# Kernel tuning notes

Measured on AMD Instinct MI355X. Metric: run time of the kernel, lower is better.

Reference implementation:

```python
import jax, jax.numpy as jnp
import numpy as np

B, N_LEAVES, HID, NCLS, VOCAB = 32, 512, 128, 2, 50257
N_NODES = 2 * N_LEAVES - 1  # complete binary tree, heap layout


def setup_inputs() -> dict:
    key = jax.random.key(0)
    ks = jax.random.split(key, 12)
    x = jax.random.randint(ks[0], (B, N_NODES), 0, VOCAB)
    cue = jax.random.randint(ks[1], (B, N_NODES), 0, NCLS)
    # word j sits at tree leaf node L-1+j
    word_index = jnp.tile(jnp.arange(N_LEAVES - 1, 2 * N_LEAVES - 1), (B, 1))
    # parent->child adjacency stored in adj[:, 1]
    A = np.zeros((2, N_NODES, N_NODES), dtype=bool)
    p = np.arange(N_LEAVES - 1)
    A[1, p, 2 * p + 1] = True
    A[1, p, 2 * p + 2] = True
    adj = jnp.asarray(np.broadcast_to(A, (B, 2, N_NODES, N_NODES)).copy())
    s = 0.05
    emb = jax.random.normal(ks[2], (VOCAB, HID - NCLS)) * s
    Wc = jax.random.normal(ks[3], (HID, 2 * HID)) * s
    bc = jax.random.normal(ks[4], (HID,)) * s
    Wd = jax.random.normal(ks[5], (2 * HID, 2 * HID)) * s
    bd = jax.random.normal(ks[6], (2 * HID,)) * s
    Wg = jax.random.normal(ks[7], (HID, HID)) * s
    bg = jax.random.normal(ks[8], (HID,)) * s
    Wcl = jax.random.normal(ks[9], (NCLS, 2 * HID)) * s
    bcl = jax.random.normal(ks[10], (NCLS,)) * s
    return dict(x=x, word_index=word_index, cue=cue, adj=adj, emb=emb,
                Wc=Wc, bc=bc, Wd=Wd, bd=bd, Wg=Wg, bg=bg, Wcl=Wcl, bcl=bcl)


def reference(x, word_index, cue, adj, emb, Wc, bc, Wd, bd, Wg, bg, Wcl, bcl):
    # adj encodes the same complete binary heap tree that is hardcoded below
    Bn, N = x.shape
    H = Wc.shape[0]
    C = bcl.shape[0]
    L = (N + 1) // 2
    depth = L.bit_length() - 1  # leaves live at level `depth`
    bidx = jnp.arange(Bn)[:, None]

    word_emb = emb[x]                                   # (B, N, H-C)
    cue_oh = jax.nn.one_hot(cue, C, dtype=word_emb.dtype)
    in_feats = jnp.concatenate([word_emb, cue_oh], -1)  # (B, N, H)
    sent = in_feats[bidx, word_index]                   # (B, L, H) leaf feats

    # ---- upward compose: level-batched bottom-up traversal ----
    h = jnp.zeros((Bn, N, H), in_feats.dtype).at[bidx, word_index].set(sent)
    for d in range(depth - 1, -1, -1):
        p = jnp.arange(2 ** d - 1, 2 ** (d + 1) - 1)
        ctx = jnp.concatenate([h[:, 2 * p + 1], h[:, 2 * p + 2]], -1)  # (B, 2^d, 2H)
        h = h.at[:, p].set(jnp.tanh(ctx @ Wc.T + bc))
    # upward_results never writes leaf rows -> leaves stay zero
    up = h.at[bidx, word_index].set(0.0)

    g_down = jax.nn.sigmoid(h[:, 0] @ Wg.T + bg)        # (B, H)

    # ---- downward decompose: level-batched top-down traversal ----
    down = jnp.zeros_like(h).at[:, 0].set(g_down)
    for d in range(depth):
        p = jnp.arange(2 ** d - 1, 2 ** (d + 1) - 1)
        ctx = jnp.concatenate([down[:, p], up[:, p]], -1)
        ch = jnp.tanh(ctx @ Wd.T + bd)                  # (B, 2^d, 2H)
        down = down.at[:, 2 * p + 1].set(ch[..., :H]).at[:, 2 * p + 2].set(ch[..., H:])

    tree = jnp.concatenate([down, up], -1)              # (B, N, 2H)
    scores = jax.nn.sigmoid(tree @ Wcl.T + bcl)
    return jax.nn.softmax(scores, -1)
```

## Files before the change

kernel.cpp:

```cpp
#include <hip/hip_runtime.h>


constexpr int NNODES = 1023;
constexpr int HB = 128;

__device__ __forceinline__ float fold16(const float* a, int l) {
  float b[8];
#pragma unroll
  for (int u = 0; u < 8; ++u) {
    const float mine = (l & 1) ? a[2 * u + 1] : a[2 * u];
    const float oth  = (l & 1) ? a[2 * u]     : a[2 * u + 1];
    b[u] = mine + __shfl_xor(oth, 1);
  }
  float c[4];
#pragma unroll
  for (int u = 0; u < 4; ++u) {
    const float mine = (l & 2) ? b[2 * u + 1] : b[2 * u];
    const float oth  = (l & 2) ? b[2 * u]     : b[2 * u + 1];
    c[u] = mine + __shfl_xor(oth, 2);
  }
  float d[2];
#pragma unroll
  for (int u = 0; u < 2; ++u) {
    const float mine = (l & 4) ? c[2 * u + 1] : c[2 * u];
    const float oth  = (l & 4) ? c[2 * u]     : c[2 * u + 1];
    d[u] = mine + __shfl_xor(oth, 4);
  }
  const float mine = (l & 8) ? d[1] : d[0];
  const float oth  = (l & 8) ? d[0] : d[1];
  return mine + __shfl_xor(oth, 8);
}

__device__ __forceinline__ float fold8(const float* a, int l) {
  float b[4];
#pragma unroll
  for (int u = 0; u < 4; ++u) {
    const float mine = (l & 1) ? a[2 * u + 1] : a[2 * u];
    const float oth  = (l & 1) ? a[2 * u]     : a[2 * u + 1];
    b[u] = mine + __shfl_xor(oth, 1);
  }
  float c[2];
#pragma unroll
  for (int u = 0; u < 2; ++u) {
    const float mine = (l & 2) ? b[2 * u + 1] : b[2 * u];
    const float oth  = (l & 2) ? b[2 * u]     : b[2 * u + 1];
    c[u] = mine + __shfl_xor(oth, 2);
  }
  const float mine = (l & 4) ? c[1] : c[0];
  const float oth  = (l & 4) ? c[0] : c[1];
  return mine + __shfl_xor(oth, 4);
}

__device__ __forceinline__ float fold4(const float* a, int l) {
  float b[2];
#pragma unroll
  for (int u = 0; u < 2; ++u) {
    const float mine = (l & 1) ? a[2 * u + 1] : a[2 * u];
    const float oth  = (l & 1) ? a[2 * u]     : a[2 * u + 1];
    b[u] = mine + __shfl_xor(oth, 1);
  }
  const float mine = (l & 2) ? b[1] : b[0];
  const float oth  = (l & 2) ? b[0] : b[1];
  return mine + __shfl_xor(oth, 2);
}

template<int CH>
__device__ __forceinline__ float foldCH(const float (&a)[CH * 4], int l16) {
  if constexpr (CH == 4) {
    return fold16(a, l16);
  } else if constexpr (CH == 2) {
    float t = fold8(a, l16);
    t += __shfl_xor(t, 8);
    return t;
  } else {
    float t = fold4(a, l16);
    t += __shfl_xor(t, 4);
    t += __shfl_xor(t, 8);
    return t;
  }
}

template<int CH>
__device__ __forceinline__ void up_pass(float* __restrict__ heap, int base, int cb,
                                        int cbase, const float4 (&w)[4][4],
                                        float bias_r, int g, int l16, bool wr) {
  float a[CH * 4];
#pragma unroll
  for (int v = 0; v < CH * 4; ++v) a[v] = 0.f;
#pragma unroll
  for (int p = 0; p < CH; ++p) {
    const float* cp = heap + (cb + 2 * (cbase + p)) * HB + l16 * 4;
#pragma unroll
    for (int m = 0; m < 4; ++m) {
      const float4 cc = *(const float4*)(cp + m * 64);
#pragma unroll
      for (int r = 0; r < 4; ++r) {
        const float4 wv = w[r][m];
        a[p * 4 + r] = fmaf(wv.x, cc.x, fmaf(wv.y, cc.y,
                        fmaf(wv.z, cc.z, fmaf(wv.w, cc.w, a[p * 4 + r]))));
      }
    }
  }
  const float tot = foldCH<CH>(a, l16);
  if (wr && l16 < CH * 4) {
    const int p = l16 >> 2;
    heap[(base + cbase + p) * HB + 4 * g + (l16 & 3)] = tanhf(tot + bias_r);
  }
}

template<int NP, int NH>
__device__ __forceinline__ void up_level16(float* __restrict__ heap,
                                           const float4 (&w)[4][4],
                                           float bias_r, int g, int l16, int ph) {
  constexpr int base = NP - 1, cb = 2 * NP - 1;
  if constexpr (NP >= 4 * NH) {
#pragma unroll
    for (int c0 = 0; c0 < NP; c0 += 4 * NH)
      up_pass<4>(heap, base, cb, c0 + ph * 4, w, bias_r, g, l16, true);
  } else if constexpr (NP * 2 == 4 * NH) {
    up_pass<2>(heap, base, cb, ph * 2, w, bias_r, g, l16, true);
  } else if constexpr (NP == NH) {
    up_pass<1>(heap, base, cb, ph, w, bias_r, g, l16, true);
  } else {
    up_pass<1>(heap, base, cb, 0, w, bias_r, g, l16, ph == 0);
  }
  __syncthreads();
}

template<int CH>
__device__ __forceinline__ void down_pass(float* __restrict__ db,
                                          const float* __restrict__ ub,
                                          int base, int cb, int cbase,
                                          const float4 (&w)[4][4],
                                          float bias_r, int g, int l16) {
  float a[CH * 4];
#pragma unroll
  for (int v = 0; v < CH * 4; ++v) a[v] = 0.f;
#pragma unroll
  for (int p = 0; p < CH; ++p) {
    const float* dp = db + (base + cbase + p) * HB + l16 * 4;
    const float* up = ub + (base + cbase + p) * HB + l16 * 4;
#pragma unroll
    for (int m = 0; m < 4; ++m) {
      const float4 cc = *(const float4*)(((m < 2) ? dp : up) + (m & 1) * 64);
#pragma unroll
      for (int r = 0; r < 4; ++r) {
        const float4 wv = w[r][m];
        a[p * 4 + r] = fmaf(wv.x, cc.x, fmaf(wv.y, cc.y,
                        fmaf(wv.z, cc.z, fmaf(wv.w, cc.w, a[p * 4 + r]))));
      }
    }
  }
  const float tot = foldCH<CH>(a, l16);
  if (l16 < CH * 4) {
    const int p = l16 >> 2;
    const int row = 4 * g + (l16 & 3);
    db[(cb + 2 * (cbase + p) + (row >> 7)) * HB + (row & 127)] = tanhf(tot + bias_r);
  }
}

template<int NP>
__device__ __forceinline__ void down_level16(float* __restrict__ db,
                                             const float* __restrict__ ub,
                                             const float4 (&w)[4][4],
                                             float bias_r, int g, int l16) {
  constexpr int base = NP - 1, cb = 2 * NP - 1;
  if constexpr (NP >= 4) {
#pragma unroll
    for (int c0 = 0; c0 < NP; c0 += 4)
      down_pass<4>(db, ub, base, cb, c0, w, bias_r, g, l16);
  } else {
    down_pass<NP>(db, ub, base, cb, 0, w, bias_r, g, l16);
  }
  __syncthreads();
}

__device__ __forceinline__ void classify16(const float* __restrict__ dn,
                                           const float* __restrict__ un,
                                           const float* __restrict__ wcl,
                                           const float* __restrict__ bcl,
                                           float* __restrict__ o, int l16) {
  const int k0 = l16 * 8;
  float s0, s1;
  {
    const float4 d0 = *(const float4*)(dn + k0);
    const float4 d1 = *(const float4*)(dn + k0 + 4);
    const float4 a0 = *(const float4*)(wcl + k0);
    const float4 a1 = *(const float4*)(wcl + k0 + 4);
    const float4 b0 = *(const float4*)(wcl + 256 + k0);
    const float4 b1 = *(const float4*)(wcl + 256 + k0 + 4);
    s0 = d0.x * a0.x + d0.y * a0.y + d0.z * a0.z + d0.w * a0.w
       + d1.x * a1.x + d1.y * a1.y + d1.z * a1.z + d1.w * a1.w;
    s1 = d0.x * b0.x + d0.y * b0.y + d0.z * b0.z + d0.w * b0.w
       + d1.x * b1.x + d1.y * b1.y + d1.z * b1.z + d1.w * b1.w;
  }
  if (un) {
    const float4 u0 = *(const float4*)(un + k0);
    const float4 u1 = *(const float4*)(un + k0 + 4);
    const float4 a0 = *(const float4*)(wcl + 128 + k0);
    const float4 a1 = *(const float4*)(wcl + 128 + k0 + 4);
    const float4 b0 = *(const float4*)(wcl + 384 + k0);
    const float4 b1 = *(const float4*)(wcl + 384 + k0 + 4);
    s0 += u0.x * a0.x + u0.y * a0.y + u0.z * a0.z + u0.w * a0.w
        + u1.x * a1.x + u1.y * a1.y + u1.z * a1.z + u1.w * a1.w;
    s1 += u0.x * b0.x + u0.y * b0.y + u0.z * b0.z + u0.w * b0.w
        + u1.x * b1.x + u1.y * b1.y + u1.z * b1.z + u1.w * b1.w;
  }
#pragma unroll
  for (int m = 8; m >= 1; m >>= 1) {
    s0 += __shfl_xor(s0, m);
    s1 += __shfl_xor(s1, m);
  }
  if (l16 == 0) {
    s0 += bcl[0]; s1 += bcl[1];
    const float p0 = 1.f / (1.f + expf(-s0));
    const float p1 = 1.f / (1.f + expf(-s1));
    const float mx = fmaxf(p0, p1);
    const float e0 = expf(p0 - mx), e1 = expf(p1 - mx);
    const float inv = 1.f / (e0 + e1);
    o[0] = e0 * inv;
    o[1] = e1 * inv;
  }
}

__global__ __launch_bounds__(512, 4) void kA_up(const int* __restrict__ x,
                                                const int* __restrict__ cue,
                                                const float* __restrict__ emb,
                                                const float* __restrict__ Wc,
                                                const float* __restrict__ bc,
                                                float* __restrict__ hw) {
  __shared__ __align__(16) float heap[63 * HB];
  __shared__ __align__(16) float pad[7296];
  const int b = blockIdx.x >> 4, s = blockIdx.x & 15, r = 15 + s;
  const int t = threadIdx.x, g = t >> 4, l16 = t & 15;
  if (t == 0) ((volatile float*)pad)[0] = 0.f;

  float4 w[4][4];
#pragma unroll
  for (int rr = 0; rr < 4; ++rr)
#pragma unroll
    for (int m = 0; m < 4; ++m)
      w[rr][m] = *(const float4*)(Wc + (4 * g + rr) * 256 + l16 * 4 + m * 64);
  const float bias_r = bc[4 * g + (l16 & 3)];

  for (int idx = t; idx < 32 * HB; idx += 512) {
    const int j = idx >> 7, k = idx & 127;
    const int gq = ((r + 1) << 5) - 1 + j;
    float v;
    if (k < 126) v = emb[(long long)x[b * NNODES + gq] * 126 + k];
    else         v = (cue[b * NNODES + gq] == (k - 126)) ? 1.f : 0.f;
    heap[(31 + j) * HB + k] = v;
  }
  __syncthreads();

  up_level16<16, 1>(heap, w, bias_r, g, l16, 0);
  up_level16<8, 1>(heap, w, bias_r, g, l16, 0);
  up_level16<4, 1>(heap, w, bias_r, g, l16, 0);
  up_level16<2, 1>(heap, w, bias_r, g, l16, 0);
  up_level16<1, 1>(heap, w, bias_r, g, l16, 0);

  float4* dst = (float4*)(hw + (size_t)(b * 16 + s) * 31 * HB);
  const float4* src = (const float4*)heap;
  for (int idx = t; idx < 31 * 32; idx += 512) dst[idx] = src[idx];
}

__global__ __launch_bounds__(1024, 4) void kB_mid(const float* __restrict__ Wc,
                                                  const float* __restrict__ bc,
                                                  const float* __restrict__ Wg,
                                                  const float* __restrict__ bg,
                                                  const float* __restrict__ Wd,
                                                  const float* __restrict__ bd,
                                                  const float* __restrict__ Wcl,
                                                  const float* __restrict__ bcl,
                                                  const float* __restrict__ hw,
                                                  float* __restrict__ dw,
                                                  float* __restrict__ out) {
  __shared__ __align__(16) float ub[31 * HB];
  __shared__ __align__(16) float db[31 * HB];
  __shared__ __align__(16) float pad[12084];
  __shared__ __align__(16) float wcl[512];
  const int b = blockIdx.x, t = threadIdx.x;
  if (t == 0) ((volatile float*)pad)[0] = 0.f;

  {
    float4* u4 = (float4*)(ub + 15 * HB);
    for (int idx = t; idx < 16 * 32; idx += 1024) {
      const int s = idx >> 5, k4 = idx & 31;
      u4[idx] = ((const float4*)(hw + (size_t)(b * 16 + s) * 31 * HB))[k4];
    }
  }
  if (t < 512) wcl[t] = Wcl[t];
  __syncthreads();

  {
    const int g = (t >> 4) & 31, l16 = t & 15, ph = t >> 9;
    float4 w[4][4];
#pragma unroll
    for (int rr = 0; rr < 4; ++rr)
#pragma unroll
      for (int m = 0; m < 4; ++m)
        w[rr][m] = *(const float4*)(Wc + (4 * g + rr) * 256 + l16 * 4 + m * 64);
    const float bias_r = bc[4 * g + (l16 & 3)];
    up_level16<8, 2>(ub, w, bias_r, g, l16, ph);
    up_level16<4, 2>(ub, w, bias_r, g, l16, ph);
    up_level16<2, 2>(ub, w, bias_r, g, l16, ph);
    up_level16<1, 2>(ub, w, bias_r, g, l16, ph);

    float4 wg[4][2];
#pragma unroll
    for (int rr = 0; rr < 4; ++rr)
#pragma unroll
      for (int m = 0; m < 2; ++m)
        wg[rr][m] = *(const float4*)(Wg + (4 * g + rr) * 128 + l16 * 4 + m * 64);
    float a[4];
#pragma unroll
    for (int v = 0; v < 4; ++v) a[v] = 0.f;
#pragma unroll
    for (int m = 0; m < 2; ++m) {
      const float4 cc = *(const float4*)(ub + l16 * 4 + m * 64);
#pragma unroll
      for (int rr = 0; rr < 4; ++rr) {
        const float4 wv = wg[rr][m];
        a[rr] = fmaf(wv.x, cc.x, fmaf(wv.y, cc.y, fmaf(wv.z, cc.z, fmaf(wv.w, cc.w, a[rr]))));
      }
    }
    float tot = fold4(a, l16);
    tot += __shfl_xor(tot, 4);
    tot += __shfl_xor(tot, 8);
    if (ph == 0 && l16 < 4) {
      const int row = 4 * g + l16;
      db[row] = 1.f / (1.f + expf(-(tot + bg[row])));
    }
    __syncthreads();
  }
  asm volatile("" ::: "memory");

  {
    const int g = t >> 4, l16 = t & 15;
    float4 w[4][4];
#pragma unroll
    for (int rr = 0; rr < 4; ++rr)
#pragma unroll
      for (int m = 0; m < 4; ++m)
        w[rr][m] = *(const float4*)(Wd + (4 * g + rr) * 256 + l16 * 4 + m * 64);
    const float bias_r = bd[4 * g + (l16 & 3)];
    down_level16<1>(db, ub, w, bias_r, g, l16);
    down_level16<2>(db, ub, w, bias_r, g, l16);
    down_level16<4>(db, ub, w, bias_r, g, l16);
    down_level16<8>(db, ub, w, bias_r, g, l16);
  }

  {
    const float4* s4 = (const float4*)(db + 15 * HB);
    float4* d4 = (float4*)dw;
    for (int idx = t; idx < 16 * 32; idx += 1024)
      d4[(size_t)b * 16 * 32 + idx] = s4[idx];
  }

  if (t < 15 * 16) {
    const int m = t >> 4;
    classify16(db + m * HB, ub + m * HB, wcl, bcl,
               out + ((size_t)b * NNODES + m) * 2, t & 15);
  }
}

__global__ __launch_bounds__(1024, 4) void kC_down(const float* __restrict__ Wd,
                                                   const float* __restrict__ bd,
                                                   const float* __restrict__ Wcl,
                                                   const float* __restrict__ bcl,
                                                   const float* __restrict__ hw,
                                                   const float* __restrict__ dw,
                                                   float* __restrict__ out) {
  __shared__ __align__(16) float ub[31 * HB];
  __shared__ __align__(16) float db[63 * HB];
  __shared__ __align__(16) float pad[7960];
  __shared__ __align__(16) float wcl[512];
  const int b = blockIdx.x >> 3, sp = blockIdx.x & 7;
  const int t = threadIdx.x, g = t >> 4, l16 = t & 15;
  if (t == 0) ((volatile float*)pad)[0] = 0.f;

  float4 w[4][4];
#pragma unroll
  for (int rr = 0; rr < 4; ++rr)
#pragma unroll
    for (int m = 0; m < 4; ++m)
      w[rr][m] = *(const float4*)(Wd + (4 * g + rr) * 256 + l16 * 4 + m * 64);
  const float bias_r = bd[4 * g + (l16 & 3)];
  if (t < 512) wcl[t] = Wcl[t];

  for (int ss = 0; ss < 2; ++ss) {
    const int s = sp * 2 + ss, r = 15 + s;

    {
      const float4* s4 = (const float4*)(hw + (size_t)(b * 16 + s) * 31 * HB);
      float4* u4 = (float4*)ub;
      for (int idx = t; idx < 31 * 32; idx += 1024) u4[idx] = s4[idx];
      const float4* dv = (const float4*)(dw + (size_t)(b * 16 + s) * HB);
      if (t < 32) ((float4*)db)[t] = dv[t];
    }
    __syncthreads();

    down_level16<1>(db, ub, w, bias_r, g, l16);
    down_level16<2>(db, ub, w, bias_r, g, l16);
    down_level16<4>(db, ub, w, bias_r, g, l16);
    down_level16<8>(db, ub, w, bias_r, g, l16);
    down_level16<16>(db, ub, w, bias_r, g, l16);

    if (t < 63 * 16) {
      const int m = t >> 4;
      const int lvl = 31 - __clz(m + 1);
      const int j = (m + 1) - (1 << lvl);
      const int gq = ((r + 1) << lvl) - 1 + j;
      classify16(db + m * HB, (m < 31) ? (ub + m * HB) : nullptr, wcl, bcl,
                 out + ((size_t)b * NNODES + gq) * 2, t & 15);
    }
    __syncthreads();
  }
}

extern "C" void kernel_launch(void* const* d_in, const int* in_sizes, int n_in,
                              void* d_out, int out_size, void* d_ws, size_t ws_size,
                              hipStream_t stream) {
  const int*   x   = (const int*)d_in[0];
  const int*   cue = (const int*)d_in[2];
  const float* emb = (const float*)d_in[4];
  const float* Wc  = (const float*)d_in[5];
  const float* bc  = (const float*)d_in[6];
  const float* Wd  = (const float*)d_in[7];
  const float* bd  = (const float*)d_in[8];
  const float* Wg  = (const float*)d_in[9];
  const float* bg  = (const float*)d_in[10];
  const float* Wcl = (const float*)d_in[11];
  const float* bcl = (const float*)d_in[12];
  float* out = (float*)d_out;

  float* hw = (float*)d_ws;
  float* dw = hw + (size_t)32 * 16 * 31 * 128;

  hipLaunchKernelGGL(kA_up,   dim3(512), dim3(512), 0, stream, x, cue, emb, Wc, bc, hw);
  hipLaunchKernelGGL(kB_mid,  dim3(32),  dim3(1024), 0, stream,
                     Wc, bc, Wg, bg, Wd, bd, Wcl, bcl, hw, dw, out);
  hipLaunchKernelGGL(kC_down, dim3(256), dim3(1024), 0, stream,
                     Wd, bd, Wcl, bcl, hw, dw, out);
}
```

Before: 80.80 us.

## Fuse mid and down kernels by recomputing the top tree in every block

Merges the single-block-per-batch mid kernel into the down kernel. Each of the eight blocks per batch element now redundantly recomputes the top up levels, the root gate and the top four down levels. Each block keeps only the two subtree-root down vectors it needs in shared memory, so the dw workspace round trip and one kernel launch go away. The cost is eight-fold redundant top-of-tree compute per batch. It also removes the low-parallelism 32-block launch that sat between the other two kernels.

```diff
diff --git a/kernel.cpp b/kernel.cpp
--- a/kernel.cpp
+++ b/kernel.cpp
@@ -264,7 +264,7 @@
   for (int idx = t; idx < 31 * 32; idx += 512) dst[idx] = src[idx];
 }
 
-__global__ __launch_bounds__(1024, 4) void kB_mid(const float* __restrict__ Wc,
+__global__ __launch_bounds__(1024, 4) void kC_all(const float* __restrict__ Wc,
                                                   const float* __restrict__ bc,
                                                   const float* __restrict__ Wg,
                                                   const float* __restrict__ bg,
@@ -273,51 +273,52 @@
                                                   const float* __restrict__ Wcl,
                                                   const float* __restrict__ bcl,
                                                   const float* __restrict__ hw,
-                                                  float* __restrict__ dw,
                                                   float* __restrict__ out) {
-  __shared__ __align__(16) float ub[31 * HB];
-  __shared__ __align__(16) float db[31 * HB];
-  __shared__ __align__(16) float pad[12084];
+  __shared__ __align__(16) float A[63 * HB];
+  __shared__ __align__(16) float B[31 * HB];
+  __shared__ __align__(16) float rootdn[2 * HB];
   __shared__ __align__(16) float wcl[512];
-  const int b = blockIdx.x, t = threadIdx.x;
+  __shared__ __align__(16) float pad[7400];
+  const int b = blockIdx.x >> 3, sp = blockIdx.x & 7;
+  const int t = threadIdx.x, g = t >> 4, l16 = t & 15;
   if (t == 0) ((volatile float*)pad)[0] = 0.f;
 
   {
-    float4* u4 = (float4*)(ub + 15 * HB);
+    float4* B4 = (float4*)(B + 15 * HB);
     for (int idx = t; idx < 16 * 32; idx += 1024) {
       const int s = idx >> 5, k4 = idx & 31;
-      u4[idx] = ((const float4*)(hw + (size_t)(b * 16 + s) * 31 * HB))[k4];
+      B4[idx] = ((const float4*)(hw + (size_t)(b * 16 + s) * 31 * HB))[k4];
     }
   }
   if (t < 512) wcl[t] = Wcl[t];
   __syncthreads();
 
   {
-    const int g = (t >> 4) & 31, l16 = t & 15, ph = t >> 9;
+    const int gu = g & 31, ph = t >> 9;
     float4 w[4][4];
 #pragma unroll
     for (int rr = 0; rr < 4; ++rr)
 #pragma unroll
       for (int m = 0; m < 4; ++m)
-        w[rr][m] = *(const float4*)(Wc + (4 * g + rr) * 256 + l16 * 4 + m * 64);
-    const float bias_r = bc[4 * g + (l16 & 3)];
-    up_level16<8, 2>(ub, w, bias_r, g, l16, ph);
-    up_level16<4, 2>(ub, w, bias_r, g, l16, ph);
-    up_level16<2, 2>(ub, w, bias_r, g, l16, ph);
-    up_level16<1, 2>(ub, w, bias_r, g, l16, ph);
+        w[rr][m] = *(const float4*)(Wc + (4 * gu + rr) * 256 + l16 * 4 + m * 64);
+    const float bias_r = bc[4 * gu + (l16 & 3)];
+    up_level16<8, 2>(B, w, bias_r, gu, l16, ph);
+    up_level16<4, 2>(B, w, bias_r, gu, l16, ph);
+    up_level16<2, 2>(B, w, bias_r, gu, l16, ph);
+    up_level16<1, 2>(B, w, bias_r, gu, l16, ph);
 
     float4 wg[4][2];
 #pragma unroll
     for (int rr = 0; rr < 4; ++rr)
 #pragma unroll
       for (int m = 0; m < 2; ++m)
-        wg[rr][m] = *(const float4*)(Wg + (4 * g + rr) * 128 + l16 * 4 + m * 64);
+        wg[rr][m] = *(const float4*)(Wg + (4 * gu + rr) * 128 + l16 * 4 + m * 64);
     float a[4];
 #pragma unroll
     for (int v = 0; v < 4; ++v) a[v] = 0.f;
 #pragma unroll
     for (int m = 0; m < 2; ++m) {
-      const float4 cc = *(const float4*)(ub + l16 * 4 + m * 64);
+      const float4 cc = *(const float4*)(B + l16 * 4 + m * 64);
 #pragma unroll
       for (int rr = 0; rr < 4; ++rr) {
         const float4 wv = wg[rr][m];
@@ -328,56 +329,12 @@
     tot += __shfl_xor(tot, 4);
     tot += __shfl_xor(tot, 8);
     if (ph == 0 && l16 < 4) {
-      const int row = 4 * g + l16;
-      db[row] = 1.f / (1.f + expf(-(tot + bg[row])));
+      const int row = 4 * gu + l16;
+      A[row] = 1.f / (1.f + expf(-(tot + bg[row])));
     }
     __syncthreads();
   }
   asm volatile("" ::: "memory");
-
-  {
-    const int g = t >> 4, l16 = t & 15;
-    float4 w[4][4];
-#pragma unroll
-    for (int rr = 0; rr < 4; ++rr)
-#pragma unroll
-      for (int m = 0; m < 4; ++m)
-        w[rr][m] = *(const float4*)(Wd + (4 * g + rr) * 256 + l16 * 4 + m * 64);
-    const float bias_r = bd[4 * g + (l16 & 3)];
-    down_level16<1>(db, ub, w, bias_r, g, l16);
-    down_level16<2>(db, ub, w, bias_r, g, l16);
-    down_level16<4>(db, ub, w, bias_r, g, l16);
-    down_level16<8>(db, ub, w, bias_r, g, l16);
-  }
-
-  {
-    const float4* s4 = (const float4*)(db + 15 * HB);
-    float4* d4 = (float4*)dw;
-    for (int idx = t; idx < 16 * 32; idx += 1024)
-      d4[(size_t)b * 16 * 32 + idx] = s4[idx];
-  }
-
-  if (t < 15 * 16) {
-    const int m = t >> 4;
-    classify16(db + m * HB, ub + m * HB, wcl, bcl,
-               out + ((size_t)b * NNODES + m) * 2, t & 15);
-  }
-}
-
-__global__ __launch_bounds__(1024, 4) void kC_down(const float* __restrict__ Wd,
-                                                   const float* __restrict__ bd,
-                                                   const float* __restrict__ Wcl,
-                                                   const float* __restrict__ bcl,
-                                                   const float* __restrict__ hw,
-                                                   const float* __restrict__ dw,
-                                                   float* __restrict__ out) {
-  __shared__ __align__(16) float ub[31 * HB];
-  __shared__ __align__(16) float db[63 * HB];
-  __shared__ __align__(16) float pad[7960];
-  __shared__ __align__(16) float wcl[512];
-  const int b = blockIdx.x >> 3, sp = blockIdx.x & 7;
-  const int t = threadIdx.x, g = t >> 4, l16 = t & 15;
-  if (t == 0) ((volatile float*)pad)[0] = 0.f;
 
   float4 w[4][4];
 #pragma unroll
@@ -386,33 +343,44 @@
     for (int m = 0; m < 4; ++m)
       w[rr][m] = *(const float4*)(Wd + (4 * g + rr) * 256 + l16 * 4 + m * 64);
   const float bias_r = bd[4 * g + (l16 & 3)];
-  if (t < 512) wcl[t] = Wcl[t];
+
+  down_level16<1>(A, B, w, bias_r, g, l16);
+  down_level16<2>(A, B, w, bias_r, g, l16);
+  down_level16<4>(A, B, w, bias_r, g, l16);
+  down_level16<8>(A, B, w, bias_r, g, l16);
+
+  if (sp == 0 && t < 15 * 16) {
+    const int m = t >> 4;
+    classify16(A + m * HB, B + m * HB, wcl, bcl,
+               out + ((size_t)b * NNODES + m) * 2, l16);
+  }
+  if (t < 256) rootdn[t] = A[(15 + sp * 2 + (t >> 7)) * HB + (t & 127)];
+  __syncthreads();
 
   for (int ss = 0; ss < 2; ++ss) {
     const int s = sp * 2 + ss, r = 15 + s;
 
     {
       const float4* s4 = (const float4*)(hw + (size_t)(b * 16 + s) * 31 * HB);
-      float4* u4 = (float4*)ub;
-      for (int idx = t; idx < 31 * 32; idx += 1024) u4[idx] = s4[idx];
-      const float4* dv = (const float4*)(dw + (size_t)(b * 16 + s) * HB);
-      if (t < 32) ((float4*)db)[t] = dv[t];
+      float4* B4 = (float4*)B;
+      for (int idx = t; idx < 31 * 32; idx += 1024) B4[idx] = s4[idx];
+      if (t < HB) A[t] = rootdn[ss * HB + t];
     }
     __syncthreads();
 
-    down_level16<1>(db, ub, w, bias_r, g, l16);
-    down_level16<2>(db, ub, w, bias_r, g, l16);
-    down_level16<4>(db, ub, w, bias_r, g, l16);
-    down_level16<8>(db, ub, w, bias_r, g, l16);
-    down_level16<16>(db, ub, w, bias_r, g, l16);
+    down_level16<1>(A, B, w, bias_r, g, l16);
+    down_level16<2>(A, B, w, bias_r, g, l16);
+    down_level16<4>(A, B, w, bias_r, g, l16);
+    down_level16<8>(A, B, w, bias_r, g, l16);
+    down_level16<16>(A, B, w, bias_r, g, l16);
 
     if (t < 63 * 16) {
       const int m = t >> 4;
       const int lvl = 31 - __clz(m + 1);
       const int j = (m + 1) - (1 << lvl);
       const int gq = ((r + 1) << lvl) - 1 + j;
-      classify16(db + m * HB, (m < 31) ? (ub + m * HB) : nullptr, wcl, bcl,
-                 out + ((size_t)b * NNODES + gq) * 2, t & 15);
+      classify16(A + m * HB, (m < 31) ? (B + m * HB) : nullptr, wcl, bcl,
+                 out + ((size_t)b * NNODES + gq) * 2, l16);
     }
     __syncthreads();
   }
@@ -435,11 +403,8 @@
   float* out = (float*)d_out;
 
   float* hw = (float*)d_ws;
-  float* dw = hw + (size_t)32 * 16 * 31 * 128;
-
-  hipLaunchKernelGGL(kA_up,   dim3(512), dim3(512), 0, stream, x, cue, emb, Wc, bc, hw);
-  hipLaunchKernelGGL(kB_mid,  dim3(32),  dim3(1024), 0, stream,
-                     Wc, bc, Wg, bg, Wd, bd, Wcl, bcl, hw, dw, out);
-  hipLaunchKernelGGL(kC_down, dim3(256), dim3(1024), 0, stream,
-                     Wd, bd, Wcl, bcl, hw, dw, out);
-}
+
+  hipLaunchKernelGGL(kA_up,  dim3(512), dim3(512), 0, stream, x, cue, emb, Wc, bc, hw);
+  hipLaunchKernelGGL(kC_all, dim3(256), dim3(1024), 0, stream,
+                     Wc, bc, Wg, bg, Wd, bd, Wcl, bcl, hw, out);
+}
```

Result: faster. 76.95 us (-4.8%).
